# Performance work log

Measured on AMD Instinct MI355X. Metric: run time of the kernel, lower is better.

The kernel has to match this reference:

```python
import jax, jax.numpy as jnp
import numpy as np

N_NODES = 50000
N_EDGES = 800000
IN_CH = 128
HID = 16
HEADS = 8
OUT_CH = 64


def setup_inputs() -> dict:
    key = jax.random.key(0)
    ks = jax.random.split(key, 16)
    H1 = HID * HEADS  # 128
    inp = {
        "x": jax.random.normal(ks[0], (N_NODES, IN_CH), dtype=jnp.float32),
        "edge_index": jax.random.randint(ks[1], (2, N_EDGES), 0, N_NODES, dtype=jnp.int64),
        # layer 1: GATv2Conv(IN_CH -> HID, heads=HEADS, concat=True)
        "W1l": jax.random.normal(ks[2], (IN_CH, H1), dtype=jnp.float32) * 0.05,
        "W1r": jax.random.normal(ks[3], (IN_CH, H1), dtype=jnp.float32) * 0.05,
        "att1": jax.random.normal(ks[4], (HEADS, HID), dtype=jnp.float32) * 0.05,
        "b1": jnp.zeros((H1,), dtype=jnp.float32),
        "skip1_W": jax.random.normal(ks[5], (IN_CH, H1), dtype=jnp.float32) * 0.05,
        "skip1_b": jnp.zeros((H1,), dtype=jnp.float32),
        # PyG LayerNorm (default mode='graph') affine params
        "ln_w": jnp.ones((H1,), dtype=jnp.float32),
        "ln_b": jnp.zeros((H1,), dtype=jnp.float32),
        # layer 2: GATv2Conv(H1 -> OUT_CH, heads=1, concat=False)
        "W2l": jax.random.normal(ks[6], (H1, OUT_CH), dtype=jnp.float32) * 0.05,
        "W2r": jax.random.normal(ks[7], (H1, OUT_CH), dtype=jnp.float32) * 0.05,
        "att2": jax.random.normal(ks[8], (1, OUT_CH), dtype=jnp.float32) * 0.05,
        "b2": jnp.zeros((OUT_CH,), dtype=jnp.float32),
        "skip2_W": jax.random.normal(ks[9], (H1, OUT_CH), dtype=jnp.float32) * 0.05,
        "skip2_b": jnp.zeros((OUT_CH,), dtype=jnp.float32),
    }
    return inp


def _gatv2(x, src, dst, Wl, Wr, att, b, concat):
    # GATv2Conv message passing (PyG semantics, share_weights=False).
    N = x.shape[0]
    H, C = att.shape
    xl = (x @ Wl).reshape(N, H, C)  # source transform (lin_l)
    xr = (x @ Wr).reshape(N, H, C)  # target transform (lin_r)
    e = jax.nn.leaky_relu(xl[src] + xr[dst], 0.2)  # [E,H,C]
    a = jnp.einsum('ehc,hc->eh', e, att)  # attention logits [E,H]
    # segment softmax over incoming edges of each dst node (self-loops guarantee non-empty)
    m = jax.lax.stop_gradient(jax.ops.segment_max(a, dst, num_segments=N))
    p = jnp.exp(a - m[dst])
    denom = jax.ops.segment_sum(p, dst, num_segments=N)
    alpha = p / denom[dst]  # [E,H]
    out = jax.ops.segment_sum(alpha[:, :, None] * xl[src], dst, num_segments=N)  # [N,H,C]
    out = out.reshape(N, H * C) if concat else out.mean(axis=1)
    return out + b


def reference(x, edge_index, W1l, W1r, att1, b1, skip1_W, skip1_b,
              ln_w, ln_b, W2l, W2r, att2, b2, skip2_W, skip2_b):
    N = x.shape[0]
    loop = jnp.arange(N, dtype=edge_index.dtype)
    src = jnp.concatenate([edge_index[0], loop])  # add_self_loops=True (PyG default)
    dst = jnp.concatenate([edge_index[1], loop])

    # layer 1: conv + skip
    h = _gatv2(x, src, dst, W1l, W1r, att1, b1, True) + (x @ skip1_W + skip1_b)
    # PyG LayerNorm, mode='graph': normalize over all nodes and features of the graph
    mu = h.mean()
    var = jnp.mean((h - mu) ** 2)
    h = ln_w * (h - mu) / jnp.sqrt(var + 1e-5) + ln_b
    h = jax.nn.elu(h)
    # dropout: inference mode -> identity

    # layer 2: conv (heads=1, concat=False) + skip
    out = _gatv2(h, src, dst, W2l, W2r, att2, b2, False) + (h @ skip2_W + skip2_b)
    return out
```

## Files before the change

### kernel.cpp

```cpp
#include <hip/hip_runtime.h>
#include <math.h>

#define NND 50000
#define NE0 800000
#define NET 850000
#define SCAN_B 196

using short8  = __attribute__((ext_vector_type(8))) short;
using ushort8 = __attribute__((ext_vector_type(8))) unsigned short;
using f32x4   = __attribute__((ext_vector_type(4))) float;

__device__ __forceinline__ float lrelu(float v) { return fmaxf(v, 0.2f * v); }

__device__ __forceinline__ unsigned short f2bf(float f) {
    unsigned int u = __float_as_uint(f);
    u = (u + 0x7fff + ((u >> 16) & 1)) >> 16;
    return (unsigned short)u;
}
__device__ __forceinline__ float2 bf2x2(unsigned int u) {
    float2 r;
    r.x = __uint_as_float(u << 16);
    r.y = __uint_as_float(u & 0xffff0000u);
    return r;
}
__device__ __forceinline__ unsigned int packbf(float x, float y) {
    return (unsigned int)f2bf(x) | ((unsigned int)f2bf(y) << 16);
}

template <int CTRL>
__device__ __forceinline__ float dpp_add(float v) {
    int j = __builtin_amdgcn_update_dpp(0, __float_as_int(v), CTRL, 0xf, 0xf, true);
    return v + __int_as_float(j);
}

__global__ __launch_bounds__(256) void wt_prep_all(
    const float* __restrict__ A0, const float* __restrict__ A1, const float* __restrict__ A2,
    const float* __restrict__ B0, const float* __restrict__ B1, const float* __restrict__ B2,
    unsigned short* __restrict__ T1, unsigned short* __restrict__ T2) {
    const int L1 = 3 * 128 * 128;
    const int L2 = 3 * 64 * 128;
    int idx = blockIdx.x * blockDim.x + threadIdx.x;
    if (idx < L1) {
        int which = idx / 16384, rem = idx - which * 16384;
        int k = rem >> 7, n = rem & 127;
        const float* S = which == 0 ? A0 : (which == 1 ? A1 : A2);
        T1[which * 16384 + n * 128 + k] = f2bf(S[rem]);
    } else if (idx < L1 + L2) {
        int idx2 = idx - L1;
        int which = idx2 / 8192, rem = idx2 - which * 8192;
        int k = rem >> 6, n = rem & 63;
        const float* S = which == 0 ? B0 : (which == 1 ? B1 : B2);
        T2[which * 8192 + n * 128 + k] = f2bf(S[rem]);
    }
}

template <int BN, bool LN, bool OUTBF>
__global__ __launch_bounds__(256) void gemm3_mfma(
    const void* __restrict__ Av,
    const unsigned short* __restrict__ Bt0, const unsigned short* __restrict__ Bt1,
    const unsigned short* __restrict__ Bt2, const float* __restrict__ bias2,
    unsigned short* __restrict__ C0, unsigned short* __restrict__ C1,
    unsigned short* __restrict__ C2b, float* __restrict__ C2f,
    const float* __restrict__ musig, const float* __restrict__ lnw,
    const float* __restrict__ lnb, int M) {
    __shared__ __align__(16) unsigned short As[64 * 128];
    const int tid = threadIdx.x;
    const int m0 = blockIdx.x * 64;

    float mu = 0.f, rinv = 1.f;
    if constexpr (LN) { mu = musig[0]; rinv = musig[1]; }

    {
        const int row = tid >> 2, qc = tid & 3;
        const int gm = m0 + row;
#pragma unroll
        for (int i = 0; i < 4; i++) {
            int k0 = qc * 32 + i * 8;
            float v[8];
            if constexpr (LN) {
                const unsigned short* A = (const unsigned short*)Av;
                if (gm < M) {
                    ushort8 us = *(const ushort8*)(A + (size_t)gm * 128 + k0);
#pragma unroll
                    for (int j = 0; j < 8; j++) v[j] = __uint_as_float((unsigned int)us[j] << 16);
                } else {
#pragma unroll
                    for (int j = 0; j < 8; j++) v[j] = 0.f;
                }
                float4 w0 = *(const float4*)(lnw + k0);
                float4 w1 = *(const float4*)(lnw + k0 + 4);
                float4 b0 = *(const float4*)(lnb + k0);
                float4 b1 = *(const float4*)(lnb + k0 + 4);
                float wv[8] = {w0.x, w0.y, w0.z, w0.w, w1.x, w1.y, w1.z, w1.w};
                float bv[8] = {b0.x, b0.y, b0.z, b0.w, b1.x, b1.y, b1.z, b1.w};
#pragma unroll
                for (int j = 0; j < 8; j++) {
                    float t = wv[j] * (v[j] - mu) * rinv + bv[j];
                    v[j] = t > 0.f ? t : __expf(t) - 1.f;
                }
            } else {
                const float* A = (const float*)Av;
                if (gm < M) {
                    float4 a0 = *(const float4*)(A + (size_t)gm * 128 + k0);
                    float4 a1 = *(const float4*)(A + (size_t)gm * 128 + k0 + 4);
                    v[0] = a0.x; v[1] = a0.y; v[2] = a0.z; v[3] = a0.w;
                    v[4] = a1.x; v[5] = a1.y; v[6] = a1.z; v[7] = a1.w;
                } else {
#pragma unroll
                    for (int j = 0; j < 8; j++) v[j] = 0.f;
                }
            }
            short8 pk;
#pragma unroll
            for (int j = 0; j < 8; j++) pk[j] = (short)f2bf(v[j]);
            *(short8*)&As[row * 128 + (k0 ^ ((row & 7) << 3))] = pk;
        }
    }
    __syncthreads();

    const int lane = tid & 63;
    const int wid = tid >> 6;
    const int lr = lane & 15;
    const int lk = lane >> 4;

    short8 a[4][4];
#pragma unroll
    for (int rf = 0; rf < 4; rf++) {
        int row = rf * 16 + lr;
#pragma unroll
        for (int kc = 0; kc < 4; kc++) {
            int k0 = kc * 32 + lk * 8;
            a[rf][kc] = *(short8*)&As[row * 128 + (k0 ^ ((row & 7) << 3))];
        }
    }

    constexpr int NCF = BN / 64;
    const int nbase = wid * (BN / 4);

    const unsigned short* Bts[3] = {Bt0, Bt1, Bt2};
#pragma unroll
    for (int j = 0; j < 3; j++) {
        const unsigned short* Bt = Bts[j];
        short8 b[NCF][4];
#pragma unroll
        for (int cf = 0; cf < NCF; cf++) {
            int n = nbase + cf * 16 + lr;
#pragma unroll
            for (int kc = 0; kc < 4; kc++)
                b[cf][kc] = *(const short8*)(Bt + (size_t)n * 128 + kc * 32 + lk * 8);
        }
        f32x4 acc[4][NCF];
#pragma unroll
        for (int rf = 0; rf < 4; rf++)
#pragma unroll
            for (int cf = 0; cf < NCF; cf++) acc[rf][cf] = (f32x4){0.f, 0.f, 0.f, 0.f};
#pragma unroll
        for (int kc = 0; kc < 4; kc++)
#pragma unroll
            for (int rf = 0; rf < 4; rf++)
#pragma unroll
                for (int cf = 0; cf < NCF; cf++)
                    acc[rf][cf] = __builtin_amdgcn_mfma_f32_16x16x32_bf16(
                        a[rf][kc], b[cf][kc], acc[rf][cf], 0, 0, 0);
        if (j < 2) {
            unsigned short* C = (j == 0) ? C0 : C1;
#pragma unroll
            for (int rf = 0; rf < 4; rf++)
#pragma unroll
                for (int cf = 0; cf < NCF; cf++) {
                    int col = nbase + cf * 16 + lr;
#pragma unroll
                    for (int r = 0; r < 4; r++) {
                        int row = m0 + rf * 16 + lk * 4 + r;
                        if (row < M) C[(size_t)row * BN + col] = f2bf(acc[rf][cf][r]);
                    }
                }
        } else {
#pragma unroll
            for (int rf = 0; rf < 4; rf++)
#pragma unroll
                for (int cf = 0; cf < NCF; cf++) {
                    int col = nbase + cf * 16 + lr;
                    float bb = bias2[col];
#pragma unroll
                    for (int r = 0; r < 4; r++) {
                        int row = m0 + rf * 16 + lk * 4 + r;
                        if (row < M) {
                            if constexpr (OUTBF)
                                C2b[(size_t)row * BN + col] = f2bf(acc[rf][cf][r] + bb);
                            else
                                C2f[(size_t)row * BN + col] = acc[rf][cf][r] + bb;
                        }
                    }
                }
        }
    }
}

__global__ __launch_bounds__(256) void csr_count(const int* __restrict__ ei, int* __restrict__ deg) {
    int i = blockIdx.x * blockDim.x + threadIdx.x;
    int stride = gridDim.x * blockDim.x;
    for (int e = i; e < NE0; e += stride) atomicAdd(&deg[ei[NE0 + e]], 1);
}

__global__ __launch_bounds__(256) void scan1(const int* __restrict__ deg,
                                             int* __restrict__ locexc,
                                             int* __restrict__ blocksum) {
    __shared__ int s[256];
    const int t = threadIdx.x;
    const int g = blockIdx.x * 256 + t;
    int v = (g < NND) ? deg[g] + 1 : 0;
    s[t] = v;
    __syncthreads();
    for (int off = 1; off < 256; off <<= 1) {
        int x = (t >= off) ? s[t - off] : 0;
        __syncthreads();
        s[t] += x;
        __syncthreads();
    }
    if (g < NND) locexc[g] = s[t] - v;
    if (t == 255) blocksum[blockIdx.x] = s[255];
}

__global__ __launch_bounds__(256) void scan2(const int* __restrict__ blocksum,
                                             int* __restrict__ blockoff,
                                             int* __restrict__ rowptr) {
    __shared__ int s[256];
    const int t = threadIdx.x;
    int v = (t < SCAN_B) ? blocksum[t] : 0;
    s[t] = v;
    __syncthreads();
    for (int off = 1; off < 256; off <<= 1) {
        int x = (t >= off) ? s[t - off] : 0;
        __syncthreads();
        s[t] += x;
        __syncthreads();
    }
    if (t < SCAN_B) blockoff[t] = s[t] - v;
    if (t == 255) rowptr[NND] = s[255];
}

__global__ __launch_bounds__(256) void scan3(const int* __restrict__ locexc,
                                             const int* __restrict__ blockoff,
                                             int* __restrict__ rowptr,
                                             int* __restrict__ csrs) {
    const int g = blockIdx.x * 256 + threadIdx.x;
    if (g < NND) {
        int rp = locexc[g] + blockoff[g >> 8];
        rowptr[g] = rp;
        csrs[rp] = g;
    }
}

__global__ __launch_bounds__(256) void csr_fill(const int* __restrict__ ei,
                                                const int* __restrict__ rowptr,
                                                int* __restrict__ cursor,
                                                int* __restrict__ csrs) {
    int i = blockIdx.x * blockDim.x + threadIdx.x;
    int stride = gridDim.x * blockDim.x;
    for (int e = i; e < NE0; e += stride) {
        int s = ei[e], d = ei[NE0 + e];
        int pos = atomicAdd(&cursor[d], 1);
        csrs[rowptr[d] + 1 + pos] = s;
    }
}

__global__ __launch_bounds__(256) void aggr_l1(const int* __restrict__ rowptr,
                                               const int* __restrict__ csrs,
                                               const unsigned short* __restrict__ xl,
                                               const unsigned short* __restrict__ xr,
                                               const float* __restrict__ att,
                                               const float* __restrict__ b1,
                                               unsigned short* __restrict__ h,
                                               float2* __restrict__ partial) {
    const int lane = threadIdx.x & 63;
    const int wv = threadIdx.x >> 6;
    int wid = (blockIdx.x * blockDim.x + threadIdx.x) >> 6;
    const int nw = (gridDim.x * blockDim.x) >> 6;
    const int c = lane * 2;
    float2 attv = *(const float2*)(att + c);
    float2 b1v = *(const float2*)(b1 + c);
    float ts = 0.f, ts2 = 0.f;
    for (int d = wid; d < NND; d += nw) {
        int p0 = rowptr[d], p1 = rowptr[d + 1];
        float2 xrv = bf2x2(*(const unsigned int*)(xr + (size_t)d * 128 + c));
        float den0 = 0.f, den1 = 0.f, den2 = 0.f, den3 = 0.f;
        float a00 = 0.f, a01 = 0.f, a10 = 0.f, a11 = 0.f;
        float a20 = 0.f, a21 = 0.f, a30 = 0.f, a31 = 0.f;
        int i = p0;
        for (; i + 4 <= p1; i += 4) {
            int s0 = csrs[i], s1 = csrs[i + 1], s2 = csrs[i + 2], s3 = csrs[i + 3];
            float2 x0 = bf2x2(*(const unsigned int*)(xl + (size_t)s0 * 128 + c));
            float2 x1 = bf2x2(*(const unsigned int*)(xl + (size_t)s1 * 128 + c));
            float2 x2 = bf2x2(*(const unsigned int*)(xl + (size_t)s2 * 128 + c));
            float2 x3 = bf2x2(*(const unsigned int*)(xl + (size_t)s3 * 128 + c));
            float q0 = lrelu(x0.x + xrv.x) * attv.x + lrelu(x0.y + xrv.y) * attv.y;
            float q1 = lrelu(x1.x + xrv.x) * attv.x + lrelu(x1.y + xrv.y) * attv.y;
            float q2 = lrelu(x2.x + xrv.x) * attv.x + lrelu(x2.y + xrv.y) * attv.y;
            float q3 = lrelu(x3.x + xrv.x) * attv.x + lrelu(x3.y + xrv.y) * attv.y;
            q0 = dpp_add<0xB1>(q0); q0 = dpp_add<0x4E>(q0); q0 = dpp_add<0x141>(q0);
            q1 = dpp_add<0xB1>(q1); q1 = dpp_add<0x4E>(q1); q1 = dpp_add<0x141>(q1);
            q2 = dpp_add<0xB1>(q2); q2 = dpp_add<0x4E>(q2); q2 = dpp_add<0x141>(q2);
            q3 = dpp_add<0xB1>(q3); q3 = dpp_add<0x4E>(q3); q3 = dpp_add<0x141>(q3);
            float p0v = __expf(q0), p1v = __expf(q1), p2v = __expf(q2), p3v = __expf(q3);
            den0 += p0v; a00 = fmaf(p0v, x0.x, a00); a01 = fmaf(p0v, x0.y, a01);
            den1 += p1v; a10 = fmaf(p1v, x1.x, a10); a11 = fmaf(p1v, x1.y, a11);
            den2 += p2v; a20 = fmaf(p2v, x2.x, a20); a21 = fmaf(p2v, x2.y, a21);
            den3 += p3v; a30 = fmaf(p3v, x3.x, a30); a31 = fmaf(p3v, x3.y, a31);
        }
        for (; i < p1; i++) {
            int s0 = csrs[i];
            float2 x0 = bf2x2(*(const unsigned int*)(xl + (size_t)s0 * 128 + c));
            float q0 = lrelu(x0.x + xrv.x) * attv.x + lrelu(x0.y + xrv.y) * attv.y;
            q0 = dpp_add<0xB1>(q0); q0 = dpp_add<0x4E>(q0); q0 = dpp_add<0x141>(q0);
            float p0v = __expf(q0);
            den0 += p0v; a00 = fmaf(p0v, x0.x, a00); a01 = fmaf(p0v, x0.y, a01);
        }
        float den = (den0 + den1) + (den2 + den3);
        float a0 = (a00 + a10) + (a20 + a30);
        float a1 = (a01 + a11) + (a21 + a31);
        float inv = 1.f / den;
        unsigned int* hp = (unsigned int*)(h + (size_t)d * 128 + c);
        float2 hv = bf2x2(*hp);
        hv.x += a0 * inv + b1v.x;
        hv.y += a1 * inv + b1v.y;
        *hp = packbf(hv.x, hv.y);
        ts += hv.x + hv.y;
        ts2 += hv.x * hv.x + hv.y * hv.y;
    }
    __shared__ float red[8];
#pragma unroll
    for (int off = 32; off; off >>= 1) {
        ts += __shfl_down(ts, off);
        ts2 += __shfl_down(ts2, off);
    }
    if (lane == 0) { red[wv * 2] = ts; red[wv * 2 + 1] = ts2; }
    __syncthreads();
    if (threadIdx.x == 0) {
        float s = red[0] + red[2] + red[4] + red[6];
        float s2 = red[1] + red[3] + red[5] + red[7];
        partial[blockIdx.x] = make_float2(s, s2);
    }
}

__global__ __launch_bounds__(256) void ln_final2(const float2* __restrict__ part, int np,
                                                 float* __restrict__ musig) {
    double s = 0.0, s2 = 0.0;
    for (int i = threadIdx.x; i < np; i += 256) {
        float2 p = part[i];
        s += p.x;
        s2 += p.y;
    }
#pragma unroll
    for (int off = 32; off; off >>= 1) {
        s += __shfl_down(s, off);
        s2 += __shfl_down(s2, off);
    }
    __shared__ double red[8];
    const int wv = threadIdx.x >> 6;
    if ((threadIdx.x & 63) == 0) { red[wv * 2] = s; red[wv * 2 + 1] = s2; }
    __syncthreads();
    if (threadIdx.x == 0) {
        double S = red[0] + red[2] + red[4] + red[6];
        double S2 = red[1] + red[3] + red[5] + red[7];
        double inv_n = 1.0 / ((double)NND * 128.0);
        double mu = S * inv_n;
        double var = S2 * inv_n - mu * mu;
        musig[0] = (float)mu;
        musig[1] = (float)(1.0 / sqrt(var + 1e-5));
    }
}

__global__ __launch_bounds__(256) void aggr_l2(const int* __restrict__ rowptr,
                                               const int* __restrict__ csrs,
                                               const unsigned short* __restrict__ xl,
                                               const unsigned short* __restrict__ xr,
                                               const float* __restrict__ att,
                                               const float* __restrict__ b2,
                                               float* __restrict__ out) {
    const int hl = threadIdx.x & 31;
    int hwid = (blockIdx.x * blockDim.x + threadIdx.x) >> 5;
    const int nhw = (gridDim.x * blockDim.x) >> 5;
    const int c = hl * 2;
    float2 attv = *(const float2*)(att + c);
    float2 b2v = *(const float2*)(b2 + c);
    for (int d = hwid; d < NND; d += nhw) {
        int p0 = rowptr[d], p1 = rowptr[d + 1];
        float2 xrv = bf2x2(*(const unsigned int*)(xr + (size_t)d * 64 + c));
        float den0 = 0.f, den1 = 0.f, den2 = 0.f, den3 = 0.f;
        float a00 = 0.f, a01 = 0.f, a10 = 0.f, a11 = 0.f;
        float a20 = 0.f, a21 = 0.f, a30 = 0.f, a31 = 0.f;
        int i = p0;
        for (; i + 4 <= p1; i += 4) {
            int s0 = csrs[i], s1 = csrs[i + 1], s2 = csrs[i + 2], s3 = csrs[i + 3];
            float2 x0 = bf2x2(*(const unsigned int*)(xl + (size_t)s0 * 64 + c));
            float2 x1 = bf2x2(*(const unsigned int*)(xl + (size_t)s1 * 64 + c));
            float2 x2 = bf2x2(*(const unsigned int*)(xl + (size_t)s2 * 64 + c));
            float2 x3 = bf2x2(*(const unsigned int*)(xl + (size_t)s3 * 64 + c));
            float q0 = lrelu(x0.x + xrv.x) * attv.x + lrelu(x0.y + xrv.y) * attv.y;
            float q1 = lrelu(x1.x + xrv.x) * attv.x + lrelu(x1.y + xrv.y) * attv.y;
            float q2 = lrelu(x2.x + xrv.x) * attv.x + lrelu(x2.y + xrv.y) * attv.y;
            float q3 = lrelu(x3.x + xrv.x) * attv.x + lrelu(x3.y + xrv.y) * attv.y;
            q0 = dpp_add<0xB1>(q0); q0 = dpp_add<0x4E>(q0); q0 = dpp_add<0x141>(q0);
            q0 = dpp_add<0x140>(q0); q0 += __shfl_xor(q0, 16);
            q1 = dpp_add<0xB1>(q1); q1 = dpp_add<0x4E>(q1); q1 = dpp_add<0x141>(q1);
            q1 = dpp_add<0x140>(q1); q1 += __shfl_xor(q1, 16);
            q2 = dpp_add<0xB1>(q2); q2 = dpp_add<0x4E>(q2); q2 = dpp_add<0x141>(q2);
            q2 = dpp_add<0x140>(q2); q2 += __shfl_xor(q2, 16);
            q3 = dpp_add<0xB1>(q3); q3 = dpp_add<0x4E>(q3); q3 = dpp_add<0x141>(q3);
            q3 = dpp_add<0x140>(q3); q3 += __shfl_xor(q3, 16);
            float p0v = __expf(q0), p1v = __expf(q1), p2v = __expf(q2), p3v = __expf(q3);
            den0 += p0v; a00 = fmaf(p0v, x0.x, a00); a01 = fmaf(p0v, x0.y, a01);
            den1 += p1v; a10 = fmaf(p1v, x1.x, a10); a11 = fmaf(p1v, x1.y, a11);
            den2 += p2v; a20 = fmaf(p2v, x2.x, a20); a21 = fmaf(p2v, x2.y, a21);
            den3 += p3v; a30 = fmaf(p3v, x3.x, a30); a31 = fmaf(p3v, x3.y, a31);
        }
        for (; i < p1; i++) {
            int s0 = csrs[i];
            float2 x0 = bf2x2(*(const unsigned int*)(xl + (size_t)s0 * 64 + c));
            float q0 = lrelu(x0.x + xrv.x) * attv.x + lrelu(x0.y + xrv.y) * attv.y;
            q0 = dpp_add<0xB1>(q0); q0 = dpp_add<0x4E>(q0); q0 = dpp_add<0x141>(q0);
            q0 = dpp_add<0x140>(q0); q0 += __shfl_xor(q0, 16);
            float p0v = __expf(q0);
            den0 += p0v; a00 = fmaf(p0v, x0.x, a00); a01 = fmaf(p0v, x0.y, a01);
        }
        float den = (den0 + den1) + (den2 + den3);
        float a0 = (a00 + a10) + (a20 + a30);
        float a1 = (a01 + a11) + (a21 + a31);
        float inv = 1.f / den;
        float2 ov = *(float2*)(out + (size_t)d * 64 + c);
        ov.x += a0 * inv + b2v.x;
        ov.y += a1 * inv + b2v.y;
        *(float2*)(out + (size_t)d * 64 + c) = ov;
    }
}

extern "C" void kernel_launch(void* const* d_in, const int* in_sizes, int n_in,
                              void* d_out, int out_size, void* d_ws, size_t ws_size,
                              hipStream_t stream) {
    (void)in_sizes; (void)n_in; (void)out_size; (void)ws_size;
    const float* x    = (const float*)d_in[0];
    const int*   ei   = (const int*)d_in[1];
    const float* W1l  = (const float*)d_in[2];
    const float* W1r  = (const float*)d_in[3];
    const float* att1 = (const float*)d_in[4];
    const float* b1   = (const float*)d_in[5];
    const float* s1W  = (const float*)d_in[6];
    const float* s1b  = (const float*)d_in[7];
    const float* lnw  = (const float*)d_in[8];
    const float* lnb  = (const float*)d_in[9];
    const float* W2l  = (const float*)d_in[10];
    const float* W2r  = (const float*)d_in[11];
    const float* att2 = (const float*)d_in[12];
    const float* b2   = (const float*)d_in[13];
    const float* s2W  = (const float*)d_in[14];
    const float* s2b  = (const float*)d_in[15];
    float* out = (float*)d_out;

    char* ws = (char*)d_ws;
    size_t off = 0;
    auto alloc = [&](size_t bytes) {
        size_t o = off;
        off = (off + bytes + 255) & ~(size_t)255;
        return o;
    };
    unsigned short* xl = (unsigned short*)(ws + alloc((size_t)NND * 128 * 2));
    unsigned short* xr = (unsigned short*)(ws + alloc((size_t)NND * 128 * 2));
    unsigned short* h  = (unsigned short*)(ws + alloc((size_t)NND * 128 * 2));
    int* deg     = (int*)(ws + alloc((size_t)NND * 4));
    int* rowptr  = (int*)(ws + alloc((size_t)(NND + 1) * 4));
    int* cursor  = (int*)(ws + alloc((size_t)NND * 4));
    int* csrs    = (int*)(ws + alloc((size_t)NET * 4));
    int* locexc  = (int*)(ws + alloc((size_t)NND * 4));
    int* blocksum= (int*)(ws + alloc((size_t)SCAN_B * 4));
    int* blockoff= (int*)(ws + alloc((size_t)SCAN_B * 4));
    unsigned short* Bt1 = (unsigned short*)(ws + alloc((size_t)3 * 128 * 128 * 2));
    unsigned short* Bt2 = (unsigned short*)(ws + alloc((size_t)3 * 64 * 128 * 2));
    float2* partial = (float2*)(ws + alloc((size_t)12500 * 8));
    float* musig = (float*)(ws + alloc(8));

    hipMemsetAsync(deg, 0, (size_t)NND * 4, stream);
    hipMemsetAsync(cursor, 0, (size_t)NND * 4, stream);

    csr_count<<<1024, 256, 0, stream>>>(ei, deg);
    scan1<<<SCAN_B, 256, 0, stream>>>(deg, locexc, blocksum);
    scan2<<<1, 256, 0, stream>>>(blocksum, blockoff, rowptr);
    scan3<<<SCAN_B, 256, 0, stream>>>(locexc, blockoff, rowptr, csrs);
    csr_fill<<<1024, 256, 0, stream>>>(ei, rowptr, cursor, csrs);

    wt_prep_all<<<288, 256, 0, stream>>>(W1l, W1r, s1W, W2l, W2r, s2W, Bt1, Bt2);

    gemm3_mfma<128, false, true><<<782, 256, 0, stream>>>(
        (const void*)x, Bt1, Bt1 + 16384, Bt1 + 32768, s1b,
        xl, xr, h, nullptr, nullptr, nullptr, nullptr, NND);
    aggr_l1<<<12500, 256, 0, stream>>>(rowptr, csrs, xl, xr, att1, b1, h, partial);
    ln_final2<<<1, 256, 0, stream>>>(partial, 12500, musig);

    gemm3_mfma<64, true, false><<<782, 256, 0, stream>>>(
        (const void*)h, Bt2, Bt2 + 8192, Bt2 + 16384, s2b,
        xl, xr, nullptr, out, musig, lnw, lnb, NND);
    aggr_l2<<<6250, 256, 0, stream>>>(rowptr, csrs, xl, xr, att2, b2, out);
}
```

Baseline: 258.3 us.

## Build CSR via two-level bucket sort with shared-memory fill

Replaces the per-edge global cursor atomics used to fill the CSR with a bucket pass. Edges are first histogrammed and scattered into 782 buckets of 64 destination nodes, packing the source id and local destination into one word. Each bucket is then placed into CSR order by one block using shared-memory cursors. This aims to localize the scattered CSR writes and atomics, but it adds two kernels, an extra 3.2 MB buffer pass, and heavily contended bucket-level global atomics.

```diff
diff --git a/kernel.cpp b/kernel.cpp
--- a/kernel.cpp
+++ b/kernel.cpp
@@ -5,6 +5,7 @@
 #define NE0 800000
 #define NET 850000
 #define SCAN_B 196
+#define NBUK 782
 
 using short8  = __attribute__((ext_vector_type(8))) short;
 using ushort8 = __attribute__((ext_vector_type(8))) unsigned short;
@@ -197,10 +198,44 @@
     }
 }
 
-__global__ __launch_bounds__(256) void csr_count(const int* __restrict__ ei, int* __restrict__ deg) {
+__global__ __launch_bounds__(256) void bhist_k(const int* __restrict__ ei,
+                                               int* __restrict__ bhist) {
     int i = blockIdx.x * blockDim.x + threadIdx.x;
     int stride = gridDim.x * blockDim.x;
-    for (int e = i; e < NE0; e += stride) atomicAdd(&deg[ei[NE0 + e]], 1);
+    for (int e = i; e < NE0; e += stride) atomicAdd(&bhist[ei[NE0 + e] >> 6], 1);
+}
+
+__global__ __launch_bounds__(1024) void bscan_k(const int* __restrict__ bhist,
+                                                int* __restrict__ bucketoff) {
+    __shared__ int s[1024];
+    const int t = threadIdx.x;
+    int v = (t < NBUK) ? bhist[t] : 0;
+    s[t] = v;
+    __syncthreads();
+    for (int off = 1; off < 1024; off <<= 1) {
+        int x = (t >= off) ? s[t - off] : 0;
+        __syncthreads();
+        s[t] += x;
+        __syncthreads();
+    }
+    if (t < NBUK) bucketoff[t] = s[t] - v;
+    if (t == NBUK - 1) bucketoff[NBUK] = s[t];
+}
+
+__global__ __launch_bounds__(256) void bscatter_k(const int* __restrict__ ei,
+                                                  const int* __restrict__ bucketoff,
+                                                  int* __restrict__ bcur,
+                                                  int* __restrict__ deg,
+                                                  unsigned int* __restrict__ buck) {
+    int i = blockIdx.x * blockDim.x + threadIdx.x;
+    int stride = gridDim.x * blockDim.x;
+    for (int e = i; e < NE0; e += stride) {
+        int s = ei[e], d = ei[NE0 + e];
+        atomicAdd(&deg[d], 1);
+        int b = d >> 6;
+        int pos = bucketoff[b] + atomicAdd(&bcur[b], 1);
+        buck[pos] = (unsigned int)s | ((unsigned int)(d & 63) << 16);
+    }
 }
 
 __global__ __launch_bounds__(256) void scan1(const int* __restrict__ deg,
@@ -252,16 +287,23 @@
     }
 }
 
-__global__ __launch_bounds__(256) void csr_fill(const int* __restrict__ ei,
-                                                const int* __restrict__ rowptr,
-                                                int* __restrict__ cursor,
-                                                int* __restrict__ csrs) {
-    int i = blockIdx.x * blockDim.x + threadIdx.x;
-    int stride = gridDim.x * blockDim.x;
-    for (int e = i; e < NE0; e += stride) {
-        int s = ei[e], d = ei[NE0 + e];
-        int pos = atomicAdd(&cursor[d], 1);
-        csrs[rowptr[d] + 1 + pos] = s;
+__global__ __launch_bounds__(256) void bfill_k(const unsigned int* __restrict__ buck,
+                                               const int* __restrict__ bucketoff,
+                                               const int* __restrict__ rowptr,
+                                               int* __restrict__ csrs) {
+    __shared__ int lcur[64];
+    const int b = blockIdx.x;
+    const int t = threadIdx.x;
+    if (t < 64) {
+        int d = b * 64 + t;
+        lcur[t] = (d < NND) ? rowptr[d] + 1 : 0;
+    }
+    __syncthreads();
+    const int start = bucketoff[b], end = bucketoff[b + 1];
+    for (int e = start + t; e < end; e += 256) {
+        unsigned int v = buck[e];
+        int pos = atomicAdd(&lcur[v >> 16], 1);
+        csrs[pos] = (int)(v & 0xffffu);
     }
 }
 
@@ -469,24 +511,30 @@
     unsigned short* h  = (unsigned short*)(ws + alloc((size_t)NND * 128 * 2));
     int* deg     = (int*)(ws + alloc((size_t)NND * 4));
     int* rowptr  = (int*)(ws + alloc((size_t)(NND + 1) * 4));
-    int* cursor  = (int*)(ws + alloc((size_t)NND * 4));
     int* csrs    = (int*)(ws + alloc((size_t)NET * 4));
     int* locexc  = (int*)(ws + alloc((size_t)NND * 4));
     int* blocksum= (int*)(ws + alloc((size_t)SCAN_B * 4));
     int* blockoff= (int*)(ws + alloc((size_t)SCAN_B * 4));
+    int* bhist   = (int*)(ws + alloc((size_t)NBUK * 4));
+    int* bucketoff=(int*)(ws + alloc((size_t)(NBUK + 1) * 4));
+    int* bcur    = (int*)(ws + alloc((size_t)NBUK * 4));
+    unsigned int* buck = (unsigned int*)(ws + alloc((size_t)NE0 * 4));
     unsigned short* Bt1 = (unsigned short*)(ws + alloc((size_t)3 * 128 * 128 * 2));
     unsigned short* Bt2 = (unsigned short*)(ws + alloc((size_t)3 * 64 * 128 * 2));
     float2* partial = (float2*)(ws + alloc((size_t)12500 * 8));
     float* musig = (float*)(ws + alloc(8));
 
     hipMemsetAsync(deg, 0, (size_t)NND * 4, stream);
-    hipMemsetAsync(cursor, 0, (size_t)NND * 4, stream);
-
-    csr_count<<<1024, 256, 0, stream>>>(ei, deg);
+    hipMemsetAsync(bhist, 0, (size_t)NBUK * 4, stream);
+    hipMemsetAsync(bcur, 0, (size_t)NBUK * 4, stream);
+
+    bhist_k<<<2048, 256, 0, stream>>>(ei, bhist);
+    bscan_k<<<1, 1024, 0, stream>>>(bhist, bucketoff);
+    bscatter_k<<<2048, 256, 0, stream>>>(ei, bucketoff, bcur, deg, buck);
     scan1<<<SCAN_B, 256, 0, stream>>>(deg, locexc, blocksum);
     scan2<<<1, 256, 0, stream>>>(blocksum, blockoff, rowptr);
     scan3<<<SCAN_B, 256, 0, stream>>>(locexc, blockoff, rowptr, csrs);
-    csr_fill<<<1024, 256, 0, stream>>>(ei, rowptr, cursor, csrs);
+    bfill_k<<<NBUK, 256, 0, stream>>>(buck, bucketoff, rowptr, csrs);
 
     wt_prep_all<<<288, 256, 0, stream>>>(W1l, W1r, s1W, W2l, W2r, s2W, Bt1, Bt2);
 
```

Measured after the change: 595.6 us. 131% more time.
